# Performance work log

Hardware: AMD Instinct MI355X
Metric: run time of the kernel (lower is better)

Reference implementation:

```python
import jax, jax.numpy as jnp
import numpy as np
from jax import lax

B, T, D, L, H, F = 2, 128, 256, 8, 4, 2048  # batch, time, dim, max_chunk_len, nhead, dim_feedforward
THRESH = 0.5


def setup_inputs() -> dict:
    key = jax.random.key(0)
    ks = jax.random.split(key, 12)
    s = 0.02
    nrm = lambda k, sh, sc=s: jax.random.normal(k, sh, jnp.float32) * sc
    return {
        "frames": jax.random.normal(ks[0], (B, T, D), jnp.float32),
        "cls_token": jax.random.normal(ks[1], (D,), jnp.float32),
        "Wq": nrm(ks[2], (D, D)), "bq": jnp.zeros((D,), jnp.float32),
        "Wk": nrm(ks[3], (D, D)), "bk": jnp.zeros((D,), jnp.float32),
        "Wv": nrm(ks[4], (D, D)), "bv": jnp.zeros((D,), jnp.float32),
        "Wo": nrm(ks[5], (D, D)), "bo": jnp.zeros((D,), jnp.float32),
        "ln1_g": jnp.ones((D,), jnp.float32), "ln1_b": jnp.zeros((D,), jnp.float32),
        "ln2_g": jnp.ones((D,), jnp.float32), "ln2_b": jnp.zeros((D,), jnp.float32),
        "W1": nrm(ks[6], (D, F)), "b1f": jnp.zeros((F,), jnp.float32),
        "W2": nrm(ks[7], (F, D)), "b2f": jnp.zeros((D,), jnp.float32),
        "We1": nrm(ks[8], (D, D)), "be1": jnp.zeros((D,), jnp.float32),
        "We2": jax.random.normal(ks[9], (D,), jnp.float32) * 0.1,
        "be2": jnp.zeros((), jnp.float32),
    }


def reference(frames, cls_token, Wq, bq, Wk, bk, Wv, bv, Wo, bo,
              ln1_g, ln1_b, ln2_g, ln2_b, W1, b1f, W2, b2f,
              We1, be1, We2, be2):
    """Dynamic chunker: for each start index i, grow window 1..L over frames[i:],
    run a pre-norm TransformerEncoderLayer on [CLS, window], stop at first
    p_eoc > THRESH (or window cap). Emits CLS encodings per chunk.
    Returns (chunks [B,T,D] zero-padded, counts [B])."""
    Bq, Tq, Dq = frames.shape
    dh = Dq // H
    scale = 1.0 / np.sqrt(dh).astype(np.float32)

    def ln(x, g, b):
        m = jnp.mean(x, -1, keepdims=True)
        v = jnp.var(x, -1, keepdims=True)
        return (x - m) * lax.rsqrt(v + 1e-5) * g + b

    def enc_cls(seq, kp):
        # seq: (1+L, D); kp: (1+L,) True = padded key. norm_first encoder layer.
        S = seq.shape[0]
        h = ln(seq, ln1_g, ln1_b)
        q = (h @ Wq + bq).reshape(S, H, dh)
        k = (h @ Wk + bk).reshape(S, H, dh)
        v = (h @ Wv + bv).reshape(S, H, dh)
        scores = jnp.einsum('qhd,khd->hqk', q, k) * scale
        scores = jnp.where(kp[None, None, :], -1e30, scores)
        a = jax.nn.softmax(scores, axis=-1)
        o = jnp.einsum('hqk,khd->qhd', a, v).reshape(S, Dq)
        x = seq + o @ Wo + bo
        h2 = ln(x, ln2_g, ln2_b)
        x = x + jax.nn.relu(h2 @ W1 + b1f) @ W2 + b2f
        return x[0]  # CLS position

    pos = jnp.arange(L)
    ls = jnp.arange(1, L + 1)

    def run(fpad):  # fpad: (T+L, D), one sample
        def step(i, _):
            win = lax.dynamic_slice(fpad, (i, 0), (L, Dq))           # frames[i:i+L] (zero-padded past T)
            seq = jnp.concatenate([cls_token[None, :], win], 0)     # (1+L, D)
            base_pad = (i + pos) >= Tq                               # positions past end of sequence
            kp = jnp.concatenate(
                [jnp.zeros((L, 1), bool),
                 (pos[None, :] >= ls[:, None]) | base_pad[None, :]], 1)  # (L, 1+L) one mask per candidate len
            enc = jax.vmap(enc_cls, in_axes=(None, 0))(seq, kp)      # (L, D) candidate CLS encodings
            p = jax.nn.sigmoid(jax.nn.relu(enc @ We1 + be1) @ We2 + be2)  # (L,) eoc probs
            lmax = jnp.clip(Tq - i, 1, L)
            stop = (p > THRESH) & (ls <= lmax)
            lstar = jnp.where(stop.any(), jnp.argmax(stop) + 1, lmax)
            active = i < Tq
            chunk = jnp.where(active, enc[lstar - 1], jnp.zeros((Dq,), seq.dtype))
            i_new = jnp.where(active, i + lstar.astype(i.dtype), i)
            return i_new, (chunk, active)

        _, (chunks, act) = lax.scan(step, jnp.int32(0), None, length=Tq)
        return chunks, act

    fpadded = jnp.pad(frames, ((0, 0), (0, L), (0, 0)))
    chunks, act = jax.vmap(run)(fpadded)
    counts = act.sum(-1).astype(jnp.int32)
    return chunks, counts
```

## Files before the change

kernel.cpp:

```cpp
#include <hip/hip_runtime.h>

#define DEV __device__ __forceinline__

constexpr int Bc = 2, Tc = 128, Dc = 256, Lc = 8, Hc = 4, DH = 64, Fc = 2048;
constexpr float EPS = 1e-5f, SCALE = 0.125f;
constexpr int NROWS = Bc * Tc * Lc;
constexpr int SLAB = NROWS * Dc;

constexpr int OFF_K     = 0;
constexpr int OFF_VWOH  = OFF_K + Bc * Tc * Dc;
constexpr int OFF_QCLS  = OFF_VWOH + Bc * Tc * Hc * Dc;
constexpr int OFF_KCLS  = OFF_QCLS + Dc;
constexpr int OFF_VWOHC = OFF_KCLS + Dc;
constexpr int OFF_ENC   = OFF_VWOHC + Hc * Dc;
constexpr int OFF_Z     = OFF_ENC + SLAB;

DEV int imin(int a, int b) { return a < b ? a : b; }

DEV float blockReduceSum(float v, float* red) {
#pragma unroll
  for (int off = 32; off; off >>= 1) v += __shfl_down(v, off, 64);
  const int lane = threadIdx.x & 63;
  const int w = threadIdx.x >> 6;
  __syncthreads();
  if (lane == 0) red[w] = v;
  __syncthreads();
  return red[0] + red[1] + red[2] + red[3];
}

__global__ __launch_bounds__(256) void k_prep(
    const float* __restrict__ frames, const float* __restrict__ cls,
    const float* __restrict__ Wq, const float* __restrict__ bq,
    const float* __restrict__ Wk, const float* __restrict__ bk,
    const float* __restrict__ Wv, const float* __restrict__ bv,
    const float* __restrict__ Wo,
    const float* __restrict__ g1, const float* __restrict__ b1,
    float* __restrict__ ws) {
  __shared__ float hsm[Dc];
  __shared__ float vsm[Dc];
  __shared__ float red[4];
  const int d = threadIdx.x;
  const int r = blockIdx.x;

  const float x = (r < Bc * Tc) ? frames[r * Dc + d] : cls[d];
  const float s = blockReduceSum(x, red);
  const float m = s * (1.0f / Dc);
  const float c = x - m;
  const float var = blockReduceSum(c * c, red) * (1.0f / Dc);
  hsm[d] = c * (1.0f / sqrtf(var + EPS)) * g1[d] + b1[d];
  __syncthreads();

  float ka = bk[d], va = bv[d];
  for (int c2 = 0; c2 < Dc; ++c2) {
    const float h = hsm[c2];
    ka = fmaf(h, Wk[c2 * Dc + d], ka);
    va = fmaf(h, Wv[c2 * Dc + d], va);
  }
  if (r < Bc * Tc) ws[OFF_K + r * Dc + d] = ka;
  else             ws[OFF_KCLS + d] = ka;
  vsm[d] = va;
  __syncthreads();

#pragma unroll
  for (int hh = 0; hh < Hc; ++hh) {
    float acc = 0.f;
    for (int c2 = 0; c2 < DH; ++c2)
      acc = fmaf(vsm[hh * DH + c2], Wo[(hh * DH + c2) * Dc + d], acc);
    if (r < Bc * Tc) ws[OFF_VWOH + r * (Hc * Dc) + hh * Dc + d] = acc;
    else             ws[OFF_VWOHC + hh * Dc + d] = acc;
  }
  if (r == Bc * Tc) {
    float qa = bq[d];
    for (int c2 = 0; c2 < Dc; ++c2) qa = fmaf(hsm[c2], Wq[c2 * Dc + d], qa);
    ws[OFF_QCLS + d] = qa;
  }
}

__global__ __launch_bounds__(512) void k_fused(
    const float* __restrict__ cls, const float* __restrict__ bo,
    const float* __restrict__ g2, const float* __restrict__ b2,
    const float* __restrict__ W1, const float* __restrict__ b1f,
    const float* __restrict__ W2, const float* __restrict__ b2f,
    const float* __restrict__ We1, const float* __restrict__ be1,
    const float* __restrict__ We2, const float* __restrict__ be2,
    float* __restrict__ ws) {
  const int wg = blockIdx.x;
  const int i = wg & (Tc - 1);
  const int tid = threadIdx.x;
  const int wv = tid >> 6, lane = tid & 63;
  const int lmax = imin(Tc - i, Lc);

  __shared__ __align__(16) float ts[8][2048];
  __shared__ __align__(16) float h2s[8][256];
  __shared__ __align__(16) float x0s[8][256];
  __shared__ __align__(16) float encs[8][256];
  __shared__ float sv[Hc][Lc + 1];
  __shared__ float aP[Lc][Hc][Lc + 1];
  __shared__ __align__(16) float redA[Lc][4];
  __shared__ __align__(16) float redB[Lc][4];
  __shared__ float zred[8][4];

  if (tid < 256) {
    const int hh = tid >> 6;
    const float qv = ws[OFF_QCLS + hh * DH + lane];
    for (int j = 0; j <= Lc; ++j) {
      float p = 0.f;
      if (j == 0) p = qv * ws[OFF_KCLS + hh * DH + lane];
      else if (j - 1 < lmax) p = qv * ws[OFF_K + (wg + j - 1) * Dc + hh * DH + lane];
#pragma unroll
      for (int off = 32; off; off >>= 1) p += __shfl_down(p, off, 64);
      if (lane == 0) sv[hh][j] = p * SCALE;
    }
  }
  __syncthreads();

  if (tid < Lc * Hc) {
    const int l = (tid >> 2) + 1, h4 = tid & 3;
    if (l <= lmax) {
      float mx = -1e30f;
      for (int j = 0; j <= l; ++j) mx = fmaxf(mx, sv[h4][j]);
      float den = 0.f;
      for (int j = 0; j <= l; ++j) den += expf(sv[h4][j] - mx);
      const float inv = 1.f / den;
      for (int j = 0; j <= l; ++j) aP[l - 1][h4][j] = expf(sv[h4][j] - mx) * inv;
    }
  }
  __syncthreads();

  float x0v[Lc];
  if (tid < 256) {
    const int d = tid;
    const float base = cls[d] + bo[d];
#pragma unroll
    for (int l = 0; l < Lc; ++l) x0v[l] = base;
    for (int j = 0; j <= lmax; ++j) {
      const float* vwp = (j == 0) ? (ws + OFF_VWOHC)
                                  : (ws + OFF_VWOH + (wg + j - 1) * (Hc * Dc));
      for (int h4 = 0; h4 < Hc; ++h4) {
        const float w = vwp[h4 * Dc + d];
        const int lstart = (j == 0) ? 1 : j;
        for (int l = lstart; l <= lmax; ++l) x0v[l - 1] = fmaf(aP[l - 1][h4][j], w, x0v[l - 1]);
      }
    }
#pragma unroll
    for (int l = 0; l < Lc; ++l) {
      float p = x0v[l];
#pragma unroll
      for (int off = 32; off; off >>= 1) p += __shfl_down(p, off, 64);
      if (lane == 0) redA[l][tid >> 6] = p;
    }
  }
  __syncthreads();

  float mean[Lc];
  if (tid < 256) {
#pragma unroll
    for (int l = 0; l < Lc; ++l) {
      const float4 s4 = *(const float4*)redA[l];
      mean[l] = (s4.x + s4.y + s4.z + s4.w) * (1.f / Dc);
    }
#pragma unroll
    for (int l = 0; l < Lc; ++l) {
      const float cv = x0v[l] - mean[l];
      float p = cv * cv;
#pragma unroll
      for (int off = 32; off; off >>= 1) p += __shfl_down(p, off, 64);
      if (lane == 0) redB[l][tid >> 6] = p;
    }
  }
  __syncthreads();

  if (tid < 256) {
    const int d = tid;
    const float g2d = g2[d], b2d = b2[d];
    for (int l = 1; l <= lmax; ++l) {
      const float4 s4 = *(const float4*)redB[l - 1];
      const float var = (s4.x + s4.y + s4.z + s4.w) * (1.f / Dc);
      const float rstd = 1.f / sqrtf(var + EPS);
      h2s[l - 1][d] = (x0v[l - 1] - mean[l - 1]) * rstd * g2d + b2d;
      x0s[l - 1][d] = x0v[l - 1];
    }
    for (int l = lmax + 1; l <= Lc; ++l) {
      h2s[l - 1][d] = 0.f;
      x0s[l - 1][d] = 0.f;
    }
  }
  __syncthreads();

  const int fg = tid * 4;
  float t[8][4];
  {
    const float4 bb = *(const float4*)&b1f[fg];
#pragma unroll
    for (int r = 0; r < 8; ++r) { t[r][0] = bb.x; t[r][1] = bb.y; t[r][2] = bb.z; t[r][3] = bb.w; }
  }
  for (int c = 0; c < Dc; c += 4) {
    float4 w1v[4];
#pragma unroll
    for (int k = 0; k < 4; ++k) w1v[k] = *(const float4*)&W1[(c + k) * Fc + fg];
#pragma unroll
    for (int r = 0; r < 8; ++r) {
      const float4 h = *(const float4*)&h2s[r][c];
      const float hv[4] = {h.x, h.y, h.z, h.w};
#pragma unroll
      for (int k = 0; k < 4; ++k) {
        t[r][0] = fmaf(hv[k], w1v[k].x, t[r][0]);
        t[r][1] = fmaf(hv[k], w1v[k].y, t[r][1]);
        t[r][2] = fmaf(hv[k], w1v[k].z, t[r][2]);
        t[r][3] = fmaf(hv[k], w1v[k].w, t[r][3]);
      }
    }
  }
#pragma unroll
  for (int r = 0; r < 8; ++r) {
    float4 v;
    v.x = fmaxf(t[r][0], 0.f); v.y = fmaxf(t[r][1], 0.f);
    v.z = fmaxf(t[r][2], 0.f); v.w = fmaxf(t[r][3], 0.f);
    *(float4*)&ts[r][fg] = v;
  }
  __syncthreads();

  const int d4 = lane * 4;
  float u[8][4];
#pragma unroll
  for (int r = 0; r < 8; ++r) { u[r][0] = 0.f; u[r][1] = 0.f; u[r][2] = 0.f; u[r][3] = 0.f; }
  for (int kk = 0; kk < 256; kk += 4) {
    const int kg = wv * 256 + kk;
    float4 w2v[4];
#pragma unroll
    for (int k = 0; k < 4; ++k) w2v[k] = *(const float4*)&W2[(kg + k) * Dc + d4];
#pragma unroll
    for (int r = 0; r < 8; ++r) {
      const float4 h = *(const float4*)&ts[r][kg];
      const float hv[4] = {h.x, h.y, h.z, h.w};
#pragma unroll
      for (int k = 0; k < 4; ++k) {
        u[r][0] = fmaf(hv[k], w2v[k].x, u[r][0]);
        u[r][1] = fmaf(hv[k], w2v[k].y, u[r][1]);
        u[r][2] = fmaf(hv[k], w2v[k].z, u[r][2]);
        u[r][3] = fmaf(hv[k], w2v[k].w, u[r][3]);
      }
    }
  }
  __syncthreads();

  float* redb = &ts[0][0];
#pragma unroll
  for (int r = 0; r < 8; ++r) {
    float4 v; v.x = u[r][0]; v.y = u[r][1]; v.z = u[r][2]; v.w = u[r][3];
    *(float4*)&redb[(wv * 8 + r) * 256 + d4] = v;
  }
  __syncthreads();

  {
    const int r = tid >> 6;
    const int dg = (tid & 63) * 4;
    float4 s = *(const float4*)&redb[(0 * 8 + r) * 256 + dg];
#pragma unroll
    for (int w = 1; w < 8; ++w) {
      const float4 p = *(const float4*)&redb[(w * 8 + r) * 256 + dg];
      s.x += p.x; s.y += p.y; s.z += p.z; s.w += p.w;
    }
    const float4 x0 = *(const float4*)&x0s[r][dg];
    const float4 bb = *(const float4*)&b2f[dg];
    float4 e;
    e.x = (x0.x + s.x) + bb.x; e.y = (x0.y + s.y) + bb.y;
    e.z = (x0.z + s.z) + bb.z; e.w = (x0.w + s.w) + bb.w;
    *(float4*)&ws[OFF_ENC + (wg * 8 + r) * Dc + dg] = e;
    *(float4*)&encs[r][dg] = e;
  }
  __syncthreads();

  {
    const int f = tid & 255;
    const int rh = tid >> 8;
    float g[4];
    const float be1f = be1[f];
#pragma unroll
    for (int rr = 0; rr < 4; ++rr) g[rr] = be1f;
    for (int c = 0; c < Dc; ++c) {
      const float w = We1[c * Dc + f];
#pragma unroll
      for (int rr = 0; rr < 4; ++rr) g[rr] = fmaf(encs[rh * 4 + rr][c], w, g[rr]);
    }
    const float w2 = We2[f];
#pragma unroll
    for (int rr = 0; rr < 4; ++rr) {
      float p = fmaxf(g[rr], 0.f) * w2;
#pragma unroll
      for (int off = 32; off; off >>= 1) p += __shfl_down(p, off, 64);
      if (lane == 0) zred[wv][rr] = p;
    }
  }
  __syncthreads();
  if (tid < 8) {
    const int r = tid;
    const int wb = (r < 4) ? 0 : 4;
    const int rl = r & 3;
    const float z = ((zred[wb + 0][rl] + zred[wb + 1][rl]) + zred[wb + 2][rl]) +
                    zred[wb + 3][rl];
    ws[OFF_Z + wg * 8 + r] = z + be2[0];
  }
}

__global__ __launch_bounds__(256) void k_emit(float* __restrict__ ws, float* __restrict__ out) {
  const int b = blockIdx.x;
  const int tid = threadIdx.x;
  __shared__ int lst[Tc];
  __shared__ int path[Tc];
  __shared__ int cnt_s;
  if (tid < Tc) {
    const int i = tid;
    const int lmax = imin(Tc - i, Lc);
    const float* z = ws + OFF_Z + (b * Tc + i) * Lc;
    int ls = lmax;
    for (int l = 1; l <= lmax; ++l) {
      if (z[l - 1] > 0.f) { ls = l; break; }
    }
    lst[tid] = ls;
  }
  __syncthreads();
  if (tid < 64) {
    const int a0 = lst[tid], a1 = lst[64 + tid];
    int cur = 0, s = 0;
    while (cur < Tc) {
      const int l = (cur < 64) ? __shfl(a0, cur, 64) : __shfl(a1, cur - 64, 64);
      if (tid == 0) path[s] = cur * Lc + l - 1;
      ++s;
      cur += l;
    }
    if (tid == 0) cnt_s = s;
  }
  __syncthreads();
  const int c = cnt_s;
  for (int s0 = 0; s0 < Tc; s0 += 8) {
    float v[8];
#pragma unroll
    for (int k = 0; k < 8; ++k) {
      const int s = s0 + k;
      v[k] = (s < c) ? ws[OFF_ENC + (b * Tc * Lc + path[s]) * Dc + tid] : 0.f;
    }
#pragma unroll
    for (int k = 0; k < 8; ++k) out[(b * Tc + s0 + k) * Dc + tid] = v[k];
  }
  if (tid == 0) out[Bc * Tc * Dc + b] = (float)c;
}

extern "C" void kernel_launch(void* const* d_in, const int* in_sizes, int n_in,
                              void* d_out, int out_size, void* d_ws, size_t ws_size,
                              hipStream_t stream) {
  const float* frames = (const float*)d_in[0];
  const float* cls    = (const float*)d_in[1];
  const float* Wq     = (const float*)d_in[2];
  const float* bq     = (const float*)d_in[3];
  const float* Wk     = (const float*)d_in[4];
  const float* bk     = (const float*)d_in[5];
  const float* Wv     = (const float*)d_in[6];
  const float* bv     = (const float*)d_in[7];
  const float* Wo     = (const float*)d_in[8];
  const float* bo     = (const float*)d_in[9];
  const float* g1     = (const float*)d_in[10];
  const float* b1     = (const float*)d_in[11];
  const float* g2     = (const float*)d_in[12];
  const float* b2     = (const float*)d_in[13];
  const float* W1     = (const float*)d_in[14];
  const float* b1f    = (const float*)d_in[15];
  const float* W2     = (const float*)d_in[16];
  const float* b2f    = (const float*)d_in[17];
  const float* We1    = (const float*)d_in[18];
  const float* be1    = (const float*)d_in[19];
  const float* We2    = (const float*)d_in[20];
  const float* be2    = (const float*)d_in[21];
  float* ws = (float*)d_ws;
  float* out = (float*)d_out;

  k_prep<<<Bc * Tc + 1, 256, 0, stream>>>(frames, cls, Wq, bq, Wk, bk, Wv, bv, Wo, g1, b1, ws);
  k_fused<<<Bc * Tc, 512, 0, stream>>>(cls, bo, g2, b2, W1, b1f, W2, b2f, We1, be1, We2, be2, ws);
  k_emit<<<Bc, 256, 0, stream>>>(ws, out);
}
```

Baseline: 227.6 us.

## Split fused encoder into attention, batched split-K FFN, and eoc-head kernels

Replaces the single per-window fused kernel with three kernels. An attention/LN2 kernel writes normalized rows to workspace. A batched FFN kernel tiles 32 rows and splits the 2048-wide hidden dimension into 8 groups, so W1/W2 loads are shared across rows and more workgroups run in parallel. A final kernel sums the partials, adds the residual and computes the eoc logit. The aim is to cut redundant weight streaming in the per-window FFN, at the cost of extra launches, large workspace partial buffers, and a fallback to the old path when the workspace is too small.

```diff
diff --git a/kernel.cpp b/kernel.cpp
--- a/kernel.cpp
+++ b/kernel.cpp
@@ -14,6 +14,12 @@
 constexpr int OFF_VWOHC = OFF_KCLS + Dc;
 constexpr int OFF_ENC   = OFF_VWOHC + Hc * Dc;
 constexpr int OFF_Z     = OFF_ENC + SLAB;
+constexpr int OFF_H2    = OFF_Z + NROWS;
+constexpr int OFF_U     = OFF_H2 + SLAB;
+
+constexpr int RB = 32;
+constexpr int GSPLIT = 8;
+constexpr int FS = Fc / GSPLIT;
 
 DEV int imin(int a, int b) { return a < b ? a : b; }
 
@@ -73,6 +79,283 @@
     float qa = bq[d];
     for (int c2 = 0; c2 < Dc; ++c2) qa = fmaf(hsm[c2], Wq[c2 * Dc + d], qa);
     ws[OFF_QCLS + d] = qa;
+  }
+}
+
+__global__ __launch_bounds__(256) void k_attn(
+    const float* __restrict__ cls, const float* __restrict__ bo,
+    const float* __restrict__ g2, const float* __restrict__ b2,
+    float* __restrict__ ws) {
+  const int wg = blockIdx.x;
+  const int i = wg & (Tc - 1);
+  const int tid = threadIdx.x;
+  const int lane = tid & 63;
+  const int lmax = imin(Tc - i, Lc);
+
+  __shared__ float sv[Hc][Lc + 1];
+  __shared__ float aP[Lc][Hc][Lc + 1];
+  __shared__ __align__(16) float redA[Lc][4];
+  __shared__ __align__(16) float redB[Lc][4];
+
+  {
+    const int hh = tid >> 6;
+    const float qv = ws[OFF_QCLS + hh * DH + lane];
+    for (int j = 0; j <= Lc; ++j) {
+      float p = 0.f;
+      if (j == 0) p = qv * ws[OFF_KCLS + hh * DH + lane];
+      else if (j - 1 < lmax) p = qv * ws[OFF_K + (wg + j - 1) * Dc + hh * DH + lane];
+#pragma unroll
+      for (int off = 32; off; off >>= 1) p += __shfl_down(p, off, 64);
+      if (lane == 0) sv[hh][j] = p * SCALE;
+    }
+  }
+  __syncthreads();
+
+  if (tid < Lc * Hc) {
+    const int l = (tid >> 2) + 1, h4 = tid & 3;
+    if (l <= lmax) {
+      float mx = -1e30f;
+      for (int j = 0; j <= l; ++j) mx = fmaxf(mx, sv[h4][j]);
+      float den = 0.f;
+      for (int j = 0; j <= l; ++j) den += expf(sv[h4][j] - mx);
+      const float inv = 1.f / den;
+      for (int j = 0; j <= l; ++j) aP[l - 1][h4][j] = expf(sv[h4][j] - mx) * inv;
+    }
+  }
+  __syncthreads();
+
+  const int d = tid;
+  float x0v[Lc];
+  {
+    const float base = cls[d] + bo[d];
+#pragma unroll
+    for (int l = 0; l < Lc; ++l) x0v[l] = base;
+    for (int j = 0; j <= lmax; ++j) {
+      const float* vwp = (j == 0) ? (ws + OFF_VWOHC)
+                                  : (ws + OFF_VWOH + (wg + j - 1) * (Hc * Dc));
+      for (int h4 = 0; h4 < Hc; ++h4) {
+        const float w = vwp[h4 * Dc + d];
+        const int lstart = (j == 0) ? 1 : j;
+        for (int l = lstart; l <= lmax; ++l) x0v[l - 1] = fmaf(aP[l - 1][h4][j], w, x0v[l - 1]);
+      }
+    }
+#pragma unroll
+    for (int l = 0; l < Lc; ++l) {
+      float p = x0v[l];
+#pragma unroll
+      for (int off = 32; off; off >>= 1) p += __shfl_down(p, off, 64);
+      if (lane == 0) redA[l][tid >> 6] = p;
+    }
+  }
+  __syncthreads();
+
+  float mean[Lc];
+  {
+#pragma unroll
+    for (int l = 0; l < Lc; ++l) {
+      const float4 s4 = *(const float4*)redA[l];
+      mean[l] = (s4.x + s4.y + s4.z + s4.w) * (1.f / Dc);
+    }
+#pragma unroll
+    for (int l = 0; l < Lc; ++l) {
+      const float cv = x0v[l] - mean[l];
+      float p = cv * cv;
+#pragma unroll
+      for (int off = 32; off; off >>= 1) p += __shfl_down(p, off, 64);
+      if (lane == 0) redB[l][tid >> 6] = p;
+    }
+  }
+  __syncthreads();
+
+  {
+    const float g2d = g2[d], b2d = b2[d];
+    for (int l = 1; l <= lmax; ++l) {
+      const float4 s4 = *(const float4*)redB[l - 1];
+      const float var = (s4.x + s4.y + s4.z + s4.w) * (1.f / Dc);
+      const float rstd = 1.f / sqrtf(var + EPS);
+      ws[OFF_H2 + (wg * Lc + l - 1) * Dc + d] = (x0v[l - 1] - mean[l - 1]) * rstd * g2d + b2d;
+      ws[OFF_ENC + (wg * Lc + l - 1) * Dc + d] = x0v[l - 1];
+    }
+    for (int l = lmax + 1; l <= Lc; ++l) {
+      ws[OFF_H2 + (wg * Lc + l - 1) * Dc + d] = 0.f;
+      ws[OFF_ENC + (wg * Lc + l - 1) * Dc + d] = 0.f;
+    }
+  }
+}
+
+__global__ __launch_bounds__(256) void k_ffn(
+    const float* __restrict__ W1, const float* __restrict__ b1f,
+    const float* __restrict__ W2, float* __restrict__ ws) {
+  const int rb = blockIdx.x >> 3;
+  const int g = blockIdx.x & 7;
+  const int r0 = rb * RB;
+  const int tid = threadIdx.x;
+  const int cg = tid & 63;
+  const int rg = tid >> 6;
+
+  __shared__ __align__(16) float h2s[RB][Dc];
+  __shared__ __align__(16) float Ts[RB][FS];
+
+#pragma unroll
+  for (int it = 0; it < 8; ++it) {
+    const int row = it * 4 + rg;
+    *(float4*)&h2s[row][cg * 4] =
+        *(const float4*)&ws[OFF_H2 + (r0 + row) * Dc + cg * 4];
+  }
+  __syncthreads();
+
+  const int f0 = g * FS + cg * 4;
+  float t[8][4];
+  {
+    const float4 bb = *(const float4*)&b1f[f0];
+#pragma unroll
+    for (int r = 0; r < 8; ++r) { t[r][0] = bb.x; t[r][1] = bb.y; t[r][2] = bb.z; t[r][3] = bb.w; }
+  }
+  {
+    const float* Wp = W1 + f0;
+    float4 wn[4];
+#pragma unroll
+    for (int k = 0; k < 4; ++k) wn[k] = *(const float4*)&Wp[k * Fc];
+    for (int c = 0; c < Dc; c += 4) {
+      float4 wc[4];
+#pragma unroll
+      for (int k = 0; k < 4; ++k) wc[k] = wn[k];
+      {
+        const float* Wn = Wp + imin(c + 4, Dc - 4) * Fc;
+#pragma unroll
+        for (int k = 0; k < 4; ++k) wn[k] = *(const float4*)&Wn[k * Fc];
+      }
+#pragma unroll
+      for (int r = 0; r < 8; ++r) {
+        const float4 h = *(const float4*)&h2s[rg * 8 + r][c];
+        const float hv[4] = {h.x, h.y, h.z, h.w};
+#pragma unroll
+        for (int k = 0; k < 4; ++k) {
+          t[r][0] = fmaf(hv[k], wc[k].x, t[r][0]);
+          t[r][1] = fmaf(hv[k], wc[k].y, t[r][1]);
+          t[r][2] = fmaf(hv[k], wc[k].z, t[r][2]);
+          t[r][3] = fmaf(hv[k], wc[k].w, t[r][3]);
+        }
+      }
+    }
+  }
+#pragma unroll
+  for (int r = 0; r < 8; ++r) {
+    float4 v;
+    v.x = fmaxf(t[r][0], 0.f); v.y = fmaxf(t[r][1], 0.f);
+    v.z = fmaxf(t[r][2], 0.f); v.w = fmaxf(t[r][3], 0.f);
+    *(float4*)&Ts[rg * 8 + r][cg * 4] = v;
+  }
+  __syncthreads();
+
+  float u[8][4];
+#pragma unroll
+  for (int r = 0; r < 8; ++r) { u[r][0] = 0.f; u[r][1] = 0.f; u[r][2] = 0.f; u[r][3] = 0.f; }
+  {
+    const float* Wp = W2 + g * FS * Dc + cg * 4;
+    float4 wn[4];
+#pragma unroll
+    for (int k = 0; k < 4; ++k) wn[k] = *(const float4*)&Wp[k * Dc];
+    for (int kk = 0; kk < FS; kk += 4) {
+      float4 wc[4];
+#pragma unroll
+      for (int k = 0; k < 4; ++k) wc[k] = wn[k];
+      {
+        const float* Wn = Wp + imin(kk + 4, FS - 4) * Dc;
+#pragma unroll
+        for (int k = 0; k < 4; ++k) wn[k] = *(const float4*)&Wn[k * Dc];
+      }
+#pragma unroll
+      for (int r = 0; r < 8; ++r) {
+        const float4 a = *(const float4*)&Ts[rg * 8 + r][kk];
+        const float av[4] = {a.x, a.y, a.z, a.w};
+#pragma unroll
+        for (int k = 0; k < 4; ++k) {
+          u[r][0] = fmaf(av[k], wc[k].x, u[r][0]);
+          u[r][1] = fmaf(av[k], wc[k].y, u[r][1]);
+          u[r][2] = fmaf(av[k], wc[k].z, u[r][2]);
+          u[r][3] = fmaf(av[k], wc[k].w, u[r][3]);
+        }
+      }
+    }
+  }
+#pragma unroll
+  for (int r = 0; r < 8; ++r) {
+    float4 v; v.x = u[r][0]; v.y = u[r][1]; v.z = u[r][2]; v.w = u[r][3];
+    *(float4*)&ws[OFF_U + (g * NROWS + r0 + rg * 8 + r) * Dc + cg * 4] = v;
+  }
+}
+
+__global__ __launch_bounds__(512) void k_z(
+    const float* __restrict__ b2f,
+    const float* __restrict__ We1, const float* __restrict__ be1,
+    const float* __restrict__ We2, const float* __restrict__ be2,
+    float* __restrict__ ws) {
+  const int wg = blockIdx.x;
+  const int tid = threadIdx.x;
+  const int wv = tid >> 6, lane = tid & 63;
+
+  __shared__ __align__(16) float encs[Lc][Dc];
+  __shared__ float zred[8][4];
+
+  {
+    const int r = tid >> 6;
+    const int dg = (tid & 63) * 4;
+    const int row = wg * Lc + r;
+    float4 s = *(const float4*)&ws[OFF_U + (0 * NROWS + row) * Dc + dg];
+#pragma unroll
+    for (int g = 1; g < GSPLIT; ++g) {
+      const float4 p = *(const float4*)&ws[OFF_U + (g * NROWS + row) * Dc + dg];
+      s.x += p.x; s.y += p.y; s.z += p.z; s.w += p.w;
+    }
+    const float4 x0 = *(const float4*)&ws[OFF_ENC + row * Dc + dg];
+    const float4 bb = *(const float4*)&b2f[dg];
+    float4 e;
+    e.x = (x0.x + s.x) + bb.x; e.y = (x0.y + s.y) + bb.y;
+    e.z = (x0.z + s.z) + bb.z; e.w = (x0.w + s.w) + bb.w;
+    *(float4*)&ws[OFF_ENC + row * Dc + dg] = e;
+    *(float4*)&encs[r][dg] = e;
+  }
+  __syncthreads();
+
+  {
+    const int f = tid & 255;
+    const int rh = tid >> 8;
+    float gr[4];
+    const float be1f = be1[f];
+#pragma unroll
+    for (int rr = 0; rr < 4; ++rr) gr[rr] = be1f;
+    for (int c = 0; c < Dc; c += 4) {
+      const float w0 = We1[(c + 0) * Dc + f];
+      const float w1 = We1[(c + 1) * Dc + f];
+      const float w2 = We1[(c + 2) * Dc + f];
+      const float w3 = We1[(c + 3) * Dc + f];
+#pragma unroll
+      for (int rr = 0; rr < 4; ++rr) {
+        const float4 e = *(const float4*)&encs[rh * 4 + rr][c];
+        gr[rr] = fmaf(e.x, w0, gr[rr]);
+        gr[rr] = fmaf(e.y, w1, gr[rr]);
+        gr[rr] = fmaf(e.z, w2, gr[rr]);
+        gr[rr] = fmaf(e.w, w3, gr[rr]);
+      }
+    }
+    const float w2v = We2[f];
+#pragma unroll
+    for (int rr = 0; rr < 4; ++rr) {
+      float p = fmaxf(gr[rr], 0.f) * w2v;
+#pragma unroll
+      for (int off = 32; off; off >>= 1) p += __shfl_down(p, off, 64);
+      if (lane == 0) zred[wv][rr] = p;
+    }
+  }
+  __syncthreads();
+  if (tid < 8) {
+    const int r = tid;
+    const int wb = (r < 4) ? 0 : 4;
+    const int rl = r & 3;
+    const float z = ((zred[wb + 0][rl] + zred[wb + 1][rl]) + zred[wb + 2][rl]) +
+                    zred[wb + 3][rl];
+    ws[OFF_Z + wg * 8 + r] = z + be2[0];
   }
 }
 
@@ -375,6 +658,14 @@
   float* out = (float*)d_out;
 
   k_prep<<<Bc * Tc + 1, 256, 0, stream>>>(frames, cls, Wq, bq, Wk, bk, Wv, bv, Wo, g1, b1, ws);
-  k_fused<<<Bc * Tc, 512, 0, stream>>>(cls, bo, g2, b2, W1, b1f, W2, b2f, We1, be1, We2, be2, ws);
+
+  const size_t need = (size_t)(OFF_U + GSPLIT * NROWS * Dc) * sizeof(float);
+  if (ws_size >= need) {
+    k_attn<<<Bc * Tc, 256, 0, stream>>>(cls, bo, g2, b2, ws);
+    k_ffn<<<(NROWS / RB) * GSPLIT, 256, 0, stream>>>(W1, b1f, W2, ws);
+    k_z<<<Bc * Tc, 512, 0, stream>>>(b2f, We1, be1, We2, be2, ws);
+  } else {
+    k_fused<<<Bc * Tc, 512, 0, stream>>>(cls, bo, g2, b2, W1, b1f, W2, b2f, We1, be1, We2, be2, ws);
+  }
   k_emit<<<Bc, 256, 0, stream>>>(ws, out);
 }
```

Result: slower. 249.4 us (+9.6%).

## Widen fused FFN kernel to 1024 threads with L2 weight prefetch warps

Applied to the files above, without the earlier changes.

Doubles the block size of the fused FFN/EOC kernel to 1024 threads. The W1 GEMM now gives each thread 2 output columns instead of 4. The W2 GEMM splits work across 16 waves by row and K-half. The We1 head processes 2 rows per thread instead of 4. The extra upper 512 threads first stream slices of W1/W2 through a dummy reduction to warm the cache. The aim is more latency hiding and parallelism per block, at the cost of higher register pressure under the 1024-thread bound and wasted bandwidth on the prefetch loads.

```diff
diff --git a/kernel.cpp b/kernel.cpp
--- a/kernel.cpp
+++ b/kernel.cpp
@@ -76,7 +76,7 @@
   }
 }
 
-__global__ __launch_bounds__(512) void k_fused(
+__global__ __launch_bounds__(1024) void k_mid(
     const float* __restrict__ cls, const float* __restrict__ bo,
     const float* __restrict__ g2, const float* __restrict__ b2,
     const float* __restrict__ W1, const float* __restrict__ b1f,
@@ -87,7 +87,7 @@
   const int wg = blockIdx.x;
   const int i = wg & (Tc - 1);
   const int tid = threadIdx.x;
-  const int wv = tid >> 6, lane = tid & 63;
+  const int lane = tid & 63;
   const int lmax = imin(Tc - i, Lc);
 
   __shared__ __align__(16) float ts[8][2048];
@@ -98,7 +98,20 @@
   __shared__ float aP[Lc][Hc][Lc + 1];
   __shared__ __align__(16) float redA[Lc][4];
   __shared__ __align__(16) float redB[Lc][4];
-  __shared__ float zred[8][4];
+  __shared__ float zred[4][4][2];
+
+  if (tid >= 512) {
+    const int chunk = (blockIdx.x >> 3) & 31;
+    const float4* src = (chunk < 16) ? (const float4*)W1 : (const float4*)W2;
+    const int base = (chunk & 15) * 8192;
+    const int t2 = tid - 512;
+    float acc = 0.f;
+    for (int it = t2; it < 8192; it += 512) {
+      const float4 a = src[base + it];
+      acc += a.x + a.y + a.z + a.w;
+    }
+    asm volatile("" ::"v"(acc));
+  }
 
   if (tid < 256) {
     const int hh = tid >> 6;
@@ -187,72 +200,77 @@
   }
   __syncthreads();
 
-  const int fg = tid * 4;
-  float t[8][4];
   {
-    const float4 bb = *(const float4*)&b1f[fg];
-#pragma unroll
-    for (int r = 0; r < 8; ++r) { t[r][0] = bb.x; t[r][1] = bb.y; t[r][2] = bb.z; t[r][3] = bb.w; }
-  }
-  for (int c = 0; c < Dc; c += 4) {
-    float4 w1v[4];
-#pragma unroll
-    for (int k = 0; k < 4; ++k) w1v[k] = *(const float4*)&W1[(c + k) * Fc + fg];
+    const int fg = tid * 2;
+    float t[8][2];
+    {
+      const float2 bb = *(const float2*)&b1f[fg];
+#pragma unroll
+      for (int r = 0; r < 8; ++r) { t[r][0] = bb.x; t[r][1] = bb.y; }
+    }
+    for (int c = 0; c < Dc; c += 4) {
+      float2 w1v[4];
+#pragma unroll
+      for (int k = 0; k < 4; ++k) w1v[k] = *(const float2*)&W1[(c + k) * Fc + fg];
+#pragma unroll
+      for (int r = 0; r < 8; ++r) {
+        const float4 h = *(const float4*)&h2s[r][c];
+        const float hv[4] = {h.x, h.y, h.z, h.w};
+#pragma unroll
+        for (int k = 0; k < 4; ++k) {
+          t[r][0] = fmaf(hv[k], w1v[k].x, t[r][0]);
+          t[r][1] = fmaf(hv[k], w1v[k].y, t[r][1]);
+        }
+      }
+    }
 #pragma unroll
     for (int r = 0; r < 8; ++r) {
-      const float4 h = *(const float4*)&h2s[r][c];
+      float2 v;
+      v.x = fmaxf(t[r][0], 0.f);
+      v.y = fmaxf(t[r][1], 0.f);
+      *(float2*)&ts[r][fg] = v;
+    }
+  }
+  __syncthreads();
+
+  const int wv16 = tid >> 6;
+  const int rw = wv16 >> 1;
+  const int kh = wv16 & 1;
+  const int d4 = lane * 4;
+  float u[4][4];
+#pragma unroll
+  for (int ch = 0; ch < 4; ++ch) { u[ch][0] = 0.f; u[ch][1] = 0.f; u[ch][2] = 0.f; u[ch][3] = 0.f; }
+#pragma unroll
+  for (int ch = 0; ch < 4; ++ch) {
+    const int kbase = kh * 1024 + ch * 256;
+    for (int kk = 0; kk < 256; kk += 4) {
+      const int kg = kbase + kk;
+      float4 w2v[4];
+#pragma unroll
+      for (int k = 0; k < 4; ++k) w2v[k] = *(const float4*)&W2[(kg + k) * Dc + d4];
+      const float4 h = *(const float4*)&ts[rw][kg];
       const float hv[4] = {h.x, h.y, h.z, h.w};
 #pragma unroll
       for (int k = 0; k < 4; ++k) {
-        t[r][0] = fmaf(hv[k], w1v[k].x, t[r][0]);
-        t[r][1] = fmaf(hv[k], w1v[k].y, t[r][1]);
-        t[r][2] = fmaf(hv[k], w1v[k].z, t[r][2]);
-        t[r][3] = fmaf(hv[k], w1v[k].w, t[r][3]);
+        u[ch][0] = fmaf(hv[k], w2v[k].x, u[ch][0]);
+        u[ch][1] = fmaf(hv[k], w2v[k].y, u[ch][1]);
+        u[ch][2] = fmaf(hv[k], w2v[k].z, u[ch][2]);
+        u[ch][3] = fmaf(hv[k], w2v[k].w, u[ch][3]);
       }
     }
   }
-#pragma unroll
-  for (int r = 0; r < 8; ++r) {
-    float4 v;
-    v.x = fmaxf(t[r][0], 0.f); v.y = fmaxf(t[r][1], 0.f);
-    v.z = fmaxf(t[r][2], 0.f); v.w = fmaxf(t[r][3], 0.f);
-    *(float4*)&ts[r][fg] = v;
-  }
-  __syncthreads();
-
-  const int d4 = lane * 4;
-  float u[8][4];
-#pragma unroll
-  for (int r = 0; r < 8; ++r) { u[r][0] = 0.f; u[r][1] = 0.f; u[r][2] = 0.f; u[r][3] = 0.f; }
-  for (int kk = 0; kk < 256; kk += 4) {
-    const int kg = wv * 256 + kk;
-    float4 w2v[4];
-#pragma unroll
-    for (int k = 0; k < 4; ++k) w2v[k] = *(const float4*)&W2[(kg + k) * Dc + d4];
-#pragma unroll
-    for (int r = 0; r < 8; ++r) {
-      const float4 h = *(const float4*)&ts[r][kg];
-      const float hv[4] = {h.x, h.y, h.z, h.w};
-#pragma unroll
-      for (int k = 0; k < 4; ++k) {
-        u[r][0] = fmaf(hv[k], w2v[k].x, u[r][0]);
-        u[r][1] = fmaf(hv[k], w2v[k].y, u[r][1]);
-        u[r][2] = fmaf(hv[k], w2v[k].z, u[r][2]);
-        u[r][3] = fmaf(hv[k], w2v[k].w, u[r][3]);
-      }
-    }
-  }
   __syncthreads();
 
   float* redb = &ts[0][0];
 #pragma unroll
-  for (int r = 0; r < 8; ++r) {
-    float4 v; v.x = u[r][0]; v.y = u[r][1]; v.z = u[r][2]; v.w = u[r][3];
-    *(float4*)&redb[(wv * 8 + r) * 256 + d4] = v;
-  }
-  __syncthreads();
-
-  {
+  for (int ch = 0; ch < 4; ++ch) {
+    const int chunkid = kh * 4 + ch;
+    float4 v; v.x = u[ch][0]; v.y = u[ch][1]; v.z = u[ch][2]; v.w = u[ch][3];
+    *(float4*)&redb[(chunkid * 8 + rw) * 256 + d4] = v;
+  }
+  __syncthreads();
+
+  if (tid < 512) {
     const int r = tid >> 6;
     const int dg = (tid & 63) * 4;
     float4 s = *(const float4*)&redb[(0 * 8 + r) * 256 + dg];
@@ -274,31 +292,31 @@
   {
     const int f = tid & 255;
     const int rh = tid >> 8;
-    float g[4];
+    const int wvl = (tid >> 6) & 3;
+    float gr[2];
     const float be1f = be1[f];
 #pragma unroll
-    for (int rr = 0; rr < 4; ++rr) g[rr] = be1f;
+    for (int rr = 0; rr < 2; ++rr) gr[rr] = be1f;
     for (int c = 0; c < Dc; ++c) {
       const float w = We1[c * Dc + f];
 #pragma unroll
-      for (int rr = 0; rr < 4; ++rr) g[rr] = fmaf(encs[rh * 4 + rr][c], w, g[rr]);
+      for (int rr = 0; rr < 2; ++rr) gr[rr] = fmaf(encs[rh * 2 + rr][c], w, gr[rr]);
     }
     const float w2 = We2[f];
 #pragma unroll
-    for (int rr = 0; rr < 4; ++rr) {
-      float p = fmaxf(g[rr], 0.f) * w2;
+    for (int rr = 0; rr < 2; ++rr) {
+      float p = fmaxf(gr[rr], 0.f) * w2;
 #pragma unroll
       for (int off = 32; off; off >>= 1) p += __shfl_down(p, off, 64);
-      if (lane == 0) zred[wv][rr] = p;
+      if (lane == 0) zred[rh][wvl][rr] = p;
     }
   }
   __syncthreads();
   if (tid < 8) {
     const int r = tid;
-    const int wb = (r < 4) ? 0 : 4;
-    const int rl = r & 3;
-    const float z = ((zred[wb + 0][rl] + zred[wb + 1][rl]) + zred[wb + 2][rl]) +
-                    zred[wb + 3][rl];
+    const int rh = r >> 1, rr = r & 1;
+    const float z = ((zred[rh][0][rr] + zred[rh][1][rr]) + zred[rh][2][rr]) +
+                    zred[rh][3][rr];
     ws[OFF_Z + wg * 8 + r] = z + be2[0];
   }
 }
@@ -375,6 +393,6 @@
   float* out = (float*)d_out;
 
   k_prep<<<Bc * Tc + 1, 256, 0, stream>>>(frames, cls, Wq, bq, Wk, bk, Wv, bv, Wo, g1, b1, ws);
-  k_fused<<<Bc * Tc, 512, 0, stream>>>(cls, bo, g2, b2, W1, b1f, W2, b2f, We1, be1, We2, be2, ws);
+  k_mid<<<Bc * Tc, 1024, 0, stream>>>(cls, bo, g2, b2, W1, b1f, W2, b2f, We1, be1, We2, be2, ws);
   k_emit<<<Bc, 256, 0, stream>>>(ws, out);
 }
```

Result: slower. 324.0 us (+42.4%).
